# Performance work log

Measured on AMD Instinct MI355X. Metric: run time of the kernel, lower is better.

## Reference

```python
import jax, jax.numpy as jnp
import numpy as np

T, B, DG, DH, S = 48, 96, 192, 384, 3
LAM, ETA = 0.9, 0.5
LN_EPS = 1e-5

def layernorm(x, g, b):
    m = jnp.mean(x, axis=-1, keepdims=True)
    v = jnp.var(x, axis=-1, keepdims=True)
    return (x - m) * jax.lax.rsqrt(v + LN_EPS) * g + b

def setup_inputs() -> dict:
    key = jax.random.key(0)
    k0, k1, k2, k3 = jax.random.split(key, 4)
    z_seq = jax.random.normal(k0, (T, B, DG), jnp.float32)
    # kaiming-uniform-ish / xavier-ish scaling for realism
    W_h = jax.random.normal(k1, (DH, DH), jnp.float32) * (2.0 / DH) ** 0.5
    W_g = jax.random.normal(k2, (DH, DG), jnp.float32) * (1.0 / DG) ** 0.5
    b_h = jnp.zeros((DH,), jnp.float32)
    ln_g = jnp.ones((DH,), jnp.float32)
    ln_b = jnp.zeros((DH,), jnp.float32)
    alpha_fw = jax.random.uniform(k3, (1,), jnp.float32)  # cfg.alpha_fw (learned scalar)
    return dict(z_seq=z_seq, W_h=W_h, W_g=W_g, b_h=b_h, ln_g=ln_g, ln_b=ln_b, alpha_fw=alpha_fw)

def reference(z_seq, W_h, W_g, b_h, ln_g, ln_b, alpha_fw):
    # compute_k(): curvature of cosine gate
    k = jnp.where(alpha_fw >= 0,
                  1.0 + jax.nn.softplus(alpha_fw),
                  1.0 / (1.0 + jax.nn.softplus(-alpha_fw)))  # shape (1,)

    def step(carry, z_t):
        h, A = carry                                   # h: [B,DH], A: [B,DH,DH]
        h_base = h @ W_h.T + z_t @ W_g.T + b_h          # [B,DH]
        h_s = jax.nn.relu(layernorm(h_base, ln_g, ln_b))
        # inner fast-weight settling loop with cosine-similarity gate
        for _ in range(S):
            Ah = jnp.einsum('bij,bj->bi', A, h_s)       # bmm(A, h)
            dot = jnp.sum(h_s * Ah, axis=-1, keepdims=True)
            n1 = jnp.maximum(jnp.linalg.norm(h_s, axis=-1, keepdims=True), 1e-6)
            n2 = jnp.maximum(jnp.linalg.norm(Ah, axis=-1, keepdims=True), 1e-6)
            R = jnp.clip(dot / (n1 * n2), 0.0, 1.0)
            a = 1.0 - (1.0 - R) ** k                    # alpha_dyn, [B,1]
            h_s = jax.nn.relu(layernorm((1.0 - a * a) * h_base + a * Ah, ln_g, ln_b))
        h = h_s
        # Hebbian fast-weight update: A <- lambda*A + eta * h h^T
        A = LAM * A + ETA * jnp.einsum('bi,bj->bij', h, h)
        return (h, A), None

    Bn, Dh = z_seq.shape[1], W_h.shape[0]
    h0 = jnp.zeros((Bn, Dh), z_seq.dtype)
    A0 = jnp.zeros((Bn, Dh, Dh), z_seq.dtype)
    (h, A), _ = jax.lax.scan(step, (h0, A0), z_seq[:-1])

    # final (query) step: no gating, no A update, h_s = relu(LN(h_base + A h_s))
    z_t = z_seq[-1]
    h_base = h @ W_h.T + z_t @ W_g.T + b_h
    h = jax.nn.relu(layernorm(h_base, ln_g, ln_b))
    for _ in range(S):
        Ah = jnp.einsum('bij,bj->bi', A, h)
        h = jax.nn.relu(layernorm(h_base + Ah, ln_g, ln_b))
    return h
```

## Files before the change

kernel.cpp:

```cpp
#include <hip/hip_runtime.h>
#include <math.h>

#define TT    48
#define BB    96
#define DG    192
#define DH    384
#define NSTEP 47
#define SETI  3
#define NT    512
#define NWAVE 8
#define NOW   6
#define NG    32
#define RPG   12
#define PREPNT 768

typedef unsigned short ushort_t;
typedef float f32x2 __attribute__((ext_vector_type(2)));

template <int CTRL, int RM>
__device__ __forceinline__ float dppadd(float acc, float x) {
  int t = __builtin_amdgcn_update_dpp(0, __float_as_int(x), CTRL, RM, 0xF, false);
  return acc + __int_as_float(t);
}

__device__ __forceinline__ float row16_sum(float v) {
  v = dppadd<0x128, 0xF>(v, v);
  v = dppadd<0x124, 0xF>(v, v);
  v = dppadd<0x122, 0xF>(v, v);
  v = dppadd<0x121, 0xF>(v, v);
  return v;
}

__device__ __forceinline__ float wave_sum63(float v) {
  v = row16_sum(v);
  v = dppadd<0x142, 0xA>(v, v);
  v = dppadd<0x143, 0xC>(v, v);
  return v;
}

__device__ __forceinline__ float blo(unsigned u) {
  return __uint_as_float(u << 16);
}
__device__ __forceinline__ float bhi(unsigned u) {
  return __uint_as_float(u & 0xFFFF0000u);
}
__device__ __forceinline__ f32x2 pkfma(f32x2 a, f32x2 b, f32x2 c) {
  return __builtin_elementwise_fma(a, b, c);
}

__device__ __forceinline__ void matvec_full(
    const ushort_t* __restrict__ Wh_b,
    const float* __restrict__ hs, const float* __restrict__ gzs,
    float* __restrict__ hbs, float& s1, float& s2,
    int g, int lane16, bool with_h)
{
  f32x2 h2[12];
  if (with_h) {
    const float4* h4 = (const float4*)hs;
#pragma unroll
    for (int c = 0; c < 6; ++c) {
      float4 hh = h4[lane16 + 16 * c];
      h2[2 * c]     = f32x2{hh.x, hh.y};
      h2[2 * c + 1] = f32x2{hh.z, hh.w};
    }
  }
#pragma unroll 2
  for (int p = 0; p < RPG; ++p) {
    const int r = g + NG * p;
    f32x2 a0 = {0.f, 0.f}, a1 = {0.f, 0.f};
    if (with_h) {
      const uint2* wh = (const uint2*)Wh_b + (size_t)r * (DH / 4);
#pragma unroll
      for (int c = 0; c < 6; ++c) {
        uint2 u = wh[lane16 + 16 * c];
        a0 = pkfma(f32x2{blo(u.x), bhi(u.x)}, h2[2 * c], a0);
        a1 = pkfma(f32x2{blo(u.y), bhi(u.y)}, h2[2 * c + 1], a1);
      }
    }
    float acc = row16_sum((a0.x + a1.x) + (a0.y + a1.y));
    if (lane16 == 0) {
      float vv = acc + gzs[r];
      hbs[r] = vv;
      s1 += vv;
      s2 += vv * vv;
    }
  }
}

__device__ __forceinline__ void matvec_ref(
    const float* __restrict__ Wh_f, const float* __restrict__ Wg_f,
    const float* __restrict__ hs, const float* __restrict__ zsh,
    const float (&bias)[RPG], float* __restrict__ hbs,
    float& s1, float& s2, int g, int lane16, bool with_h)
{
  f32x2 h2[12];
  if (with_h) {
    const float4* h4 = (const float4*)hs;
#pragma unroll
    for (int c = 0; c < 6; ++c) {
      float4 hh = h4[lane16 + 16 * c];
      h2[2 * c]     = f32x2{hh.x, hh.y};
      h2[2 * c + 1] = f32x2{hh.z, hh.w};
    }
  }
  float4 zz[3];
  const float4* z4 = (const float4*)zsh;
#pragma unroll
  for (int c = 0; c < 3; ++c) zz[c] = z4[lane16 + 16 * c];
#pragma unroll 2
  for (int p = 0; p < RPG; ++p) {
    const int r = g + NG * p;
    f32x2 a0 = {0.f, 0.f}, a1 = {0.f, 0.f};
    const float4* wg = (const float4*)Wg_f + (size_t)r * (DG / 4);
#pragma unroll
    for (int c = 0; c < 3; ++c) {
      float4 w = wg[lane16 + 16 * c];
      a0 = pkfma(f32x2{w.x, w.y}, f32x2{zz[c].x, zz[c].y}, a0);
      a1 = pkfma(f32x2{w.z, w.w}, f32x2{zz[c].z, zz[c].w}, a1);
    }
    if (with_h) {
      const float4* wh = (const float4*)Wh_f + (size_t)r * (DH / 4);
#pragma unroll
      for (int c = 0; c < 6; ++c) {
        float4 w = wh[lane16 + 16 * c];
        a0 = pkfma(f32x2{w.x, w.y}, h2[2 * c], a0);
        a1 = pkfma(f32x2{w.z, w.w}, h2[2 * c + 1], a1);
      }
    }
    float acc = row16_sum((a0.x + a1.x) + (a0.y + a1.y));
    if (lane16 == 0) {
      float vv = acc + bias[p];
      hbs[r] = vv;
      s1 += vv;
      s2 += vv * vv;
    }
  }
}

template <bool FULL>
__global__ __launch_bounds__(NT, 2) void fw_rnn_kernel(
    const float* __restrict__ z_seq,
    const float* __restrict__ Wh_f,
    const float* __restrict__ Wg_f,
    const ushort_t* __restrict__ Wh_b,
    const float* __restrict__ gz,
    const float* __restrict__ b_h,
    const float* __restrict__ ln_g,
    const float* __restrict__ ln_b,
    const float* __restrict__ alpha_fw,
    float* __restrict__ out)
{
  __shared__ __align__(16) float hs[DH];
  __shared__ __align__(16) float hbs[DH];
  __shared__ __align__(16) float gzs[DH];
  __shared__ __align__(16) float zsh[DG];
  __shared__ float wlam[NSTEP];
  __shared__ __align__(16) float carr[48];
  __shared__ __align__(16) float redA[NWAVE * 2];
  __shared__ __align__(16) float redB[2][32];

  const int tid    = threadIdx.x;
  const int b      = blockIdx.x;
  const int lane   = tid & 63, wv = tid >> 6;
  const int g      = tid >> 4, lane16 = tid & 15;
  const bool owner = (tid < DH);
  const bool zst   = (!FULL) && (tid >= DH) && (tid < DH + DG / 4);

  float bias[RPG];
#pragma unroll
  for (int p = 0; p < RPG; ++p) bias[p] = 0.f;
  if (!FULL && lane16 == 0) {
#pragma unroll
    for (int p = 0; p < RPG; ++p) bias[p] = b_h[g + NG * p];
  }
  float g_i = 0.f, be_i = 0.f;
  if (owner) { g_i = ln_g[tid]; be_i = ln_b[tid]; }

  const float af   = alpha_fw[0];
  const float kcur = (af >= 0.f) ? (1.f + log1pf(expf(af)))
                                 : (1.f / (1.f + log1pf(expf(-af))));
  const float invD = 1.0f / (float)DH;

  float hcol[48];
#pragma unroll
  for (int q = 0; q < 48; ++q) hcol[q] = 0.f;
  float4 hregA[6], hregB[6];
#pragma unroll
  for (int c = 0; c < 6; ++c) {
    hregA[c] = float4{0.f, 0.f, 0.f, 0.f};
    hregB[c] = float4{0.f, 0.f, 0.f, 0.f};
  }

  if (FULL && tid < DH / 4)
    ((float4*)gzs)[tid] = ((const float4*)(gz + (size_t)b * DH))[tid];
  if (!FULL && tid < DG / 4)
    ((float4*)zsh)[tid] = ((const float4*)(z_seq + (size_t)b * DG))[tid];
  if (tid < 48) carr[tid] = 0.f;
  if (tid < 2) { redB[tid][30] = 0.f; redB[tid][31] = 0.f; }
  __syncthreads();

  float Shb = 0.f, Shb2 = 0.f;

  for (int t = 0; t < NSTEP; ++t) {
    float4 gzn = {0.f, 0.f, 0.f, 0.f};
    if (FULL && tid < DH / 4)
      gzn = ((const float4*)(gz + ((size_t)(t + 1) * BB + b) * DH))[tid];

    float s1 = 0.f, s2 = 0.f;
    if (FULL)
      matvec_full(Wh_b, hs, gzs, hbs, s1, s2, g, lane16, t > 0);
    else
      matvec_ref(Wh_f, Wg_f, hs, zsh, bias, hbs, s1, s2, g, lane16, t > 0);

    if (t > 0) {
      if (g == t - 1) {
#pragma unroll
        for (int c = 0; c < 6; ++c) hregA[c] = ((const float4*)hs)[lane16 + 16 * c];
      }
      if (g + NG == t - 1) {
#pragma unroll
        for (int c = 0; c < 6; ++c) hregB[c] = ((const float4*)hs)[lane16 + 16 * c];
      }
    }
    {
      float v0 = wave_sum63(s1);
      float v1 = wave_sum63(s2);
      if (lane == 63) { redA[wv * 2] = v0; redA[wv * 2 + 1] = v1; }
    }
    __syncthreads();

    float hb = 0.f, hsv = 0.f;
    if (owner) {
      float S1 = 0.f, S2 = 0.f;
      const float4* ra4 = (const float4*)redA;
#pragma unroll
      for (int q = 0; q < 4; ++q) {
        float4 ch = ra4[q];
        S1 += ch.x + ch.z;
        S2 += ch.y + ch.w;
      }
      Shb = S1; Shb2 = S2;
      hb = hbs[tid];
      float m   = S1 * invD;
      float var = S2 * invD - m * m;
      hsv = fmaxf((hb - m) * rsqrtf(var + 1e-5f) * g_i + be_i, 0.f);
      hs[tid] = hsv;
    }
    if (t == 0) {
      if (owner) hcol[0] = hsv;
      if (tid == 0) wlam[0] = 0.5f;
      if (FULL && tid < DH / 4) ((float4*)gzs)[tid] = gzn;
      if (zst)
        ((float4*)zsh)[tid - DH] =
            ((const float4*)(z_seq + ((size_t)1 * BB + b) * DG))[tid - DH];
      __syncthreads();
      continue;
    }
    __syncthreads();

    float4 znext;
    if (zst)
      znext = ((const float4*)(z_seq + ((size_t)(t + 1) * BB + b) * DG))[tid - DH];

    for (int s = 0; s < SETI; ++s) {
      if (g < t) {
        float4 ss[6];
        const float4* s4 = (const float4*)hs;
#pragma unroll
        for (int c = 0; c < 6; ++c) ss[c] = s4[lane16 + 16 * c];
        {
          f32x2 p0 = {0.f, 0.f}, p1 = {0.f, 0.f};
#pragma unroll
          for (int c = 0; c < 6; ++c) {
            p0 = pkfma(f32x2{hregA[c].x, hregA[c].y}, f32x2{ss[c].x, ss[c].y}, p0);
            p1 = pkfma(f32x2{hregA[c].z, hregA[c].w}, f32x2{ss[c].z, ss[c].w}, p1);
          }
          float p = row16_sum((p0.x + p1.x) + (p0.y + p1.y));
          if (lane16 == 0) carr[g] = p * wlam[g];
        }
        if (g + NG < t) {
          f32x2 p0 = {0.f, 0.f}, p1 = {0.f, 0.f};
#pragma unroll
          for (int c = 0; c < 6; ++c) {
            p0 = pkfma(f32x2{hregB[c].x, hregB[c].y}, f32x2{ss[c].x, ss[c].y}, p0);
            p1 = pkfma(f32x2{hregB[c].z, hregB[c].w}, f32x2{ss[c].z, ss[c].w}, p1);
          }
          float p = row16_sum((p0.x + p1.x) + (p0.y + p1.y));
          if (lane16 == 0) carr[g + NG] = p * wlam[g + NG];
        }
      }
      __syncthreads();

      float ah = 0.f;
      if (owner) {
        const float4* c4 = (const float4*)carr;
        float a0 = 0.f, a1 = 0.f, a2 = 0.f, a3 = 0.f;
#pragma unroll
        for (int q = 0; q < 12; ++q) {
          float4 cc = c4[q];
          a0 = fmaf(cc.x, hcol[4 * q + 0], a0);
          a1 = fmaf(cc.y, hcol[4 * q + 1], a1);
          a2 = fmaf(cc.z, hcol[4 * q + 2], a2);
          a3 = fmaf(cc.w, hcol[4 * q + 3], a3);
        }
        ah = (a0 + a2) + (a1 + a3);
        float v0 = wave_sum63(hsv * ah);
        float v1 = wave_sum63(hsv * hsv);
        float v2 = wave_sum63(ah * ah);
        float v3 = wave_sum63(hb * ah);
        float v4 = wave_sum63(ah);
        if (lane == 63) {
          float* rb = redB[s & 1];
          rb[wv * 5 + 0] = v0; rb[wv * 5 + 1] = v1; rb[wv * 5 + 2] = v2;
          rb[wv * 5 + 3] = v3; rb[wv * 5 + 4] = v4;
        }
      }
      __syncthreads();

      if (owner) {
        const float4* rb4 = (const float4*)redB[s & 1];
        float S[5] = {0.f, 0.f, 0.f, 0.f, 0.f};
#pragma unroll
        for (int q = 0; q < 8; ++q) {
          float4 ch = rb4[q];
          S[(4 * q + 0) % 5] += ch.x;
          S[(4 * q + 1) % 5] += ch.y;
          S[(4 * q + 2) % 5] += ch.z;
          S[(4 * q + 3) % 5] += ch.w;
        }
        float n1 = fmaxf(sqrtf(S[1]), 1e-6f);
        float n2 = fmaxf(sqrtf(S[2]), 1e-6f);
        float R  = fminf(fmaxf(__fdividef(S[0], n1 * n2), 0.f), 1.f);
        float a  = 1.f - __expf(kcur * __logf(1.f - R));
        float beta = 1.f - a * a;
        float mu  = (beta * Shb + a * S[4]) * invD;
        float Exx = (beta * beta * Shb2 + 2.f * beta * a * S[3] + a * a * S[2]) * invD;
        float var = Exx - mu * mu;
        float xv  = beta * hb + a * ah;
        hsv = fmaxf((xv - mu) * rsqrtf(var + 1e-5f) * g_i + be_i, 0.f);
        hs[tid] = hsv;
        if (s == SETI - 1) {
#pragma unroll
          for (int q = 0; q < 48; ++q)
            if (q == t) hcol[q] = hsv;
        }
      }
      if (s == SETI - 1) {
        if (tid < t) wlam[tid] *= 0.9f;
        else if (tid == t) wlam[tid] = 0.5f;
        if (FULL && tid < DH / 4) ((float4*)gzs)[tid] = gzn;
        if (zst) ((float4*)zsh)[tid - DH] = znext;
      }
      __syncthreads();
    }
  }

  {
    float s1 = 0.f, s2 = 0.f;
    if (FULL)
      matvec_full(Wh_b, hs, gzs, hbs, s1, s2, g, lane16, true);
    else
      matvec_ref(Wh_f, Wg_f, hs, zsh, bias, hbs, s1, s2, g, lane16, true);
    if (g + NG == NSTEP - 1) {
#pragma unroll
      for (int c = 0; c < 6; ++c) hregB[c] = ((const float4*)hs)[lane16 + 16 * c];
    }
    {
      float v0 = wave_sum63(s1);
      float v1 = wave_sum63(s2);
      if (lane == 63) { redA[wv * 2] = v0; redA[wv * 2 + 1] = v1; }
    }
    __syncthreads();

    float hb = 0.f, hv = 0.f;
    if (owner) {
      float S1 = 0.f, S2 = 0.f;
      const float4* ra4 = (const float4*)redA;
#pragma unroll
      for (int q = 0; q < 4; ++q) {
        float4 ch = ra4[q];
        S1 += ch.x + ch.z;
        S2 += ch.y + ch.w;
      }
      Shb = S1; Shb2 = S2;
      hb = hbs[tid];
      float m   = S1 * invD;
      float var = S2 * invD - m * m;
      hv = fmaxf((hb - m) * rsqrtf(var + 1e-5f) * g_i + be_i, 0.f);
      hs[tid] = hv;
    }
    __syncthreads();

    for (int s = 0; s < SETI; ++s) {
      {
        float4 ss[6];
        const float4* s4 = (const float4*)hs;
#pragma unroll
        for (int c = 0; c < 6; ++c) ss[c] = s4[lane16 + 16 * c];
        {
          f32x2 p0 = {0.f, 0.f}, p1 = {0.f, 0.f};
#pragma unroll
          for (int c = 0; c < 6; ++c) {
            p0 = pkfma(f32x2{hregA[c].x, hregA[c].y}, f32x2{ss[c].x, ss[c].y}, p0);
            p1 = pkfma(f32x2{hregA[c].z, hregA[c].w}, f32x2{ss[c].z, ss[c].w}, p1);
          }
          float p = row16_sum((p0.x + p1.x) + (p0.y + p1.y));
          if (lane16 == 0) carr[g] = p * wlam[g];
        }
        if (g + NG < NSTEP) {
          f32x2 p0 = {0.f, 0.f}, p1 = {0.f, 0.f};
#pragma unroll
          for (int c = 0; c < 6; ++c) {
            p0 = pkfma(f32x2{hregB[c].x, hregB[c].y}, f32x2{ss[c].x, ss[c].y}, p0);
            p1 = pkfma(f32x2{hregB[c].z, hregB[c].w}, f32x2{ss[c].z, ss[c].w}, p1);
          }
          float p = row16_sum((p0.x + p1.x) + (p0.y + p1.y));
          if (lane16 == 0) carr[g + NG] = p * wlam[g + NG];
        }
      }
      __syncthreads();

      float ah = 0.f;
      if (owner) {
        const float4* c4 = (const float4*)carr;
        float a0 = 0.f, a1 = 0.f, a2 = 0.f, a3 = 0.f;
#pragma unroll
        for (int q = 0; q < 12; ++q) {
          float4 cc = c4[q];
          a0 = fmaf(cc.x, hcol[4 * q + 0], a0);
          a1 = fmaf(cc.y, hcol[4 * q + 1], a1);
          a2 = fmaf(cc.z, hcol[4 * q + 2], a2);
          a3 = fmaf(cc.w, hcol[4 * q + 3], a3);
        }
        ah = (a0 + a2) + (a1 + a3);
        float v0 = wave_sum63(ah);
        float v1 = wave_sum63(ah * ah);
        float v2 = wave_sum63(hb * ah);
        if (lane == 63) {
          float* rb = redB[s & 1];
          rb[wv * 5 + 0] = v0; rb[wv * 5 + 1] = v1; rb[wv * 5 + 2] = v2;
        }
      }
      __syncthreads();

      if (owner) {
        const float4* rb4 = (const float4*)redB[s & 1];
        float S[5] = {0.f, 0.f, 0.f, 0.f, 0.f};
#pragma unroll
        for (int q = 0; q < 8; ++q) {
          float4 ch = rb4[q];
          S[(4 * q + 0) % 5] += ch.x;
          S[(4 * q + 1) % 5] += ch.y;
          S[(4 * q + 2) % 5] += ch.z;
          S[(4 * q + 3) % 5] += ch.w;
        }
        float Sx  = Shb + S[0];
        float Sxx = Shb2 + 2.f * S[2] + S[1];
        float mu  = Sx * invD;
        float var = Sxx * invD - mu * mu;
        float xv  = hb + ah;
        hv = fmaxf((xv - mu) * rsqrtf(var + 1e-5f) * g_i + be_i, 0.f);
        if (s < SETI - 1) hs[tid] = hv;
      }
      if (s < SETI - 1) __syncthreads();
    }

    if (owner) out[(size_t)b * DH + tid] = hv;
  }
}

__global__ __launch_bounds__(PREPNT) void prep_kernel(
    const float* __restrict__ z_seq, const float* __restrict__ Wg,
    const float* __restrict__ W_h, const float* __restrict__ b_h,
    ushort_t* __restrict__ Whb, float* __restrict__ gz)
{
  __shared__ __align__(16) float zsh[DG];
  const int tid = threadIdx.x, b = blockIdx.x;
  const int g = tid >> 4, lane16 = tid & 15;

  {
    int lid = (blockIdx.y * BB + blockIdx.x) * PREPNT + tid;
    if (lid < DH * DH) {
      unsigned u = __float_as_uint(W_h[lid]);
      unsigned r = (u + 0x7FFFu + ((u >> 16) & 1u)) >> 16;
      Whb[lid] = (ushort_t)r;
    }
  }

  float4 w[24];
#pragma unroll
  for (int p = 0; p < 8; ++p)
#pragma unroll
    for (int c = 0; c < 3; ++c)
      w[p * 3 + c] = ((const float4*)Wg)[(size_t)(8 * g + p) * (DG / 4) + lane16 + 16 * c];
  float4 bs0 = {0.f, 0.f, 0.f, 0.f}, bs1 = {0.f, 0.f, 0.f, 0.f};
  if (lane16 == 0) {
    bs0 = ((const float4*)b_h)[2 * g];
    bs1 = ((const float4*)b_h)[2 * g + 1];
  }
  for (int tt = 0; tt < 6; ++tt) {
    const int t = blockIdx.y * 6 + tt;
    __syncthreads();
    if (tid < DG / 4)
      ((float4*)zsh)[tid] = ((const float4*)(z_seq + ((size_t)t * BB + b) * DG))[tid];
    __syncthreads();
    float4 zz[3];
#pragma unroll
    for (int c = 0; c < 3; ++c) zz[c] = ((const float4*)zsh)[lane16 + 16 * c];
    float rs[8];
#pragma unroll
    for (int p = 0; p < 8; ++p) {
      f32x2 a0 = {0.f, 0.f}, a1 = {0.f, 0.f};
#pragma unroll
      for (int c = 0; c < 3; ++c) {
        a0 = pkfma(f32x2{w[p * 3 + c].x, w[p * 3 + c].y}, f32x2{zz[c].x, zz[c].y}, a0);
        a1 = pkfma(f32x2{w[p * 3 + c].z, w[p * 3 + c].w}, f32x2{zz[c].z, zz[c].w}, a1);
      }
      rs[p] = row16_sum((a0.x + a1.x) + (a0.y + a1.y));
    }
    if (lane16 == 0) {
      float* grow = gz + ((size_t)t * BB + b) * DH + 8 * g;
      ((float4*)grow)[0] = float4{rs[0] + bs0.x, rs[1] + bs0.y, rs[2] + bs0.z, rs[3] + bs0.w};
      ((float4*)grow)[1] = float4{rs[4] + bs1.x, rs[5] + bs1.y, rs[6] + bs1.z, rs[7] + bs1.w};
    }
  }
}

extern "C" void kernel_launch(void* const* d_in, const int* in_sizes, int n_in,
                              void* d_out, int out_size, void* d_ws, size_t ws_size,
                              hipStream_t stream) {
  const float* z_seq    = (const float*)d_in[0];
  const float* W_h      = (const float*)d_in[1];
  const float* W_g      = (const float*)d_in[2];
  const float* b_h      = (const float*)d_in[3];
  const float* ln_g     = (const float*)d_in[4];
  const float* ln_b     = (const float*)d_in[5];
  const float* alpha_fw = (const float*)d_in[6];
  float* out = (float*)d_out;

  const size_t nWh = (size_t)DH * DH;
  const size_t bf16Bytes = nWh * sizeof(ushort_t);
  const size_t gzBytes   = (size_t)TT * BB * DH * sizeof(float);

  if (ws_size >= bf16Bytes + gzBytes) {
    ushort_t* Whb = (ushort_t*)d_ws;
    float* gz = (float*)((char*)d_ws + bf16Bytes);
    prep_kernel<<<dim3(BB, 8), dim3(PREPNT), 0, stream>>>(
        z_seq, W_g, W_h, b_h, Whb, gz);
    fw_rnn_kernel<true><<<dim3(BB), dim3(NT), 0, stream>>>(
        z_seq, W_h, W_g, Whb, gz, b_h, ln_g, ln_b, alpha_fw, out);
  } else {
    fw_rnn_kernel<false><<<dim3(BB), dim3(NT), 0, stream>>>(
        z_seq, W_h, W_g, nullptr, nullptr, b_h, ln_g, ln_b, alpha_fw, out);
  }
}
```

Before: 545.5 us.

## Stage half of bf16 W_h in LDS and prefetch the rest into registers

```diff
diff --git a/kernel.cpp b/kernel.cpp
--- a/kernel.cpp
+++ b/kernel.cpp
@@ -12,6 +12,8 @@
 #define NOW   6
 #define NG    32
 #define RPG   12
+#define LWROWS 192
+#define LWSTR  97
 #define PREPNT 768
 
 typedef unsigned short ushort_t;
@@ -48,14 +50,34 @@
   return __builtin_elementwise_fma(a, b, c);
 }
 
+__device__ __forceinline__ float rowdot(const uint2* w, const f32x2 (&h2)[12]) {
+  f32x2 a0 = {0.f, 0.f}, a1 = {0.f, 0.f};
+#pragma unroll
+  for (int c = 0; c < 6; ++c) {
+    uint2 u = w[c];
+    a0 = pkfma(f32x2{blo(u.x), bhi(u.x)}, h2[2 * c], a0);
+    a1 = pkfma(f32x2{blo(u.y), bhi(u.y)}, h2[2 * c + 1], a1);
+  }
+  return row16_sum((a0.x + a1.x) + (a0.y + a1.y));
+}
+
 __device__ __forceinline__ void matvec_full(
-    const ushort_t* __restrict__ Wh_b,
+    const uint2* __restrict__ lwh, const ushort_t* __restrict__ Wh_b,
     const float* __restrict__ hs, const float* __restrict__ gzs,
     float* __restrict__ hbs, float& s1, float& s2,
     int g, int lane16, bool with_h)
 {
-  f32x2 h2[12];
+  float rs[RPG];
   if (with_h) {
+    const uint2* wsrc = (const uint2*)Wh_b;
+    uint2 uwA[18];
+#pragma unroll
+    for (int pp = 0; pp < 3; ++pp)
+#pragma unroll
+      for (int c = 0; c < 6; ++c)
+        uwA[pp * 6 + c] =
+            wsrc[(size_t)(g + NG * (6 + pp)) * (DH / 4) + lane16 + 16 * c];
+    f32x2 h2[12];
     const float4* h4 = (const float4*)hs;
 #pragma unroll
     for (int c = 0; c < 6; ++c) {
@@ -63,23 +85,40 @@
       h2[2 * c]     = f32x2{hh.x, hh.y};
       h2[2 * c + 1] = f32x2{hh.z, hh.w};
     }
-  }
-#pragma unroll 2
-  for (int p = 0; p < RPG; ++p) {
-    const int r = g + NG * p;
-    f32x2 a0 = {0.f, 0.f}, a1 = {0.f, 0.f};
-    if (with_h) {
-      const uint2* wh = (const uint2*)Wh_b + (size_t)r * (DH / 4);
+#pragma unroll
+    for (int p = 0; p < 6; ++p) {
+      const int r = g + NG * p;
+      f32x2 a0 = {0.f, 0.f}, a1 = {0.f, 0.f};
 #pragma unroll
       for (int c = 0; c < 6; ++c) {
-        uint2 u = wh[lane16 + 16 * c];
+        uint2 u = lwh[r * LWSTR + lane16 + 16 * c];
         a0 = pkfma(f32x2{blo(u.x), bhi(u.x)}, h2[2 * c], a0);
         a1 = pkfma(f32x2{blo(u.y), bhi(u.y)}, h2[2 * c + 1], a1);
       }
-    }
-    float acc = row16_sum((a0.x + a1.x) + (a0.y + a1.y));
-    if (lane16 == 0) {
-      float vv = acc + gzs[r];
+      rs[p] = row16_sum((a0.x + a1.x) + (a0.y + a1.y));
+    }
+    uint2 uwB[18];
+#pragma unroll
+    for (int pp = 0; pp < 3; ++pp)
+#pragma unroll
+      for (int c = 0; c < 6; ++c)
+        uwB[pp * 6 + c] =
+            wsrc[(size_t)(g + NG * (9 + pp)) * (DH / 4) + lane16 + 16 * c];
+    rs[6] = rowdot(uwA, h2);
+    rs[7] = rowdot(uwA + 6, h2);
+    rs[8] = rowdot(uwA + 12, h2);
+    rs[9]  = rowdot(uwB, h2);
+    rs[10] = rowdot(uwB + 6, h2);
+    rs[11] = rowdot(uwB + 12, h2);
+  } else {
+#pragma unroll
+    for (int p = 0; p < RPG; ++p) rs[p] = 0.f;
+  }
+  if (lane16 == 0) {
+#pragma unroll
+    for (int p = 0; p < RPG; ++p) {
+      const int r = g + NG * p;
+      float vv = rs[p] + gzs[r];
       hbs[r] = vv;
       s1 += vv;
       s2 += vv * vv;
@@ -150,6 +189,7 @@
     const float* __restrict__ alpha_fw,
     float* __restrict__ out)
 {
+  __shared__ __align__(16) uint2 lwh[LWROWS * LWSTR];
   __shared__ __align__(16) float hs[DH];
   __shared__ __align__(16) float hbs[DH];
   __shared__ __align__(16) float gzs[DH];
@@ -166,6 +206,14 @@
   const bool owner = (tid < DH);
   const bool zst   = (!FULL) && (tid >= DH) && (tid < DH + DG / 4);
 
+  if (FULL) {
+    const uint2* src = (const uint2*)Wh_b;
+    for (int i = tid; i < LWROWS * 96; i += NT) {
+      int row = i / 96, col = i - 96 * (i / 96);
+      lwh[row * LWSTR + col] = src[(size_t)row * 96 + col];
+    }
+  }
+
   float bias[RPG];
 #pragma unroll
   for (int p = 0; p < RPG; ++p) bias[p] = 0.f;
@@ -208,7 +256,7 @@
 
     float s1 = 0.f, s2 = 0.f;
     if (FULL)
-      matvec_full(Wh_b, hs, gzs, hbs, s1, s2, g, lane16, t > 0);
+      matvec_full(lwh, Wh_b, hs, gzs, hbs, s1, s2, g, lane16, t > 0);
     else
       matvec_ref(Wh_f, Wg_f, hs, zsh, bias, hbs, s1, s2, g, lane16, t > 0);
 
@@ -358,7 +406,7 @@
   {
     float s1 = 0.f, s2 = 0.f;
     if (FULL)
-      matvec_full(Wh_b, hs, gzs, hbs, s1, s2, g, lane16, true);
+      matvec_full(lwh, Wh_b, hs, gzs, hbs, s1, s2, g, lane16, true);
     else
       matvec_ref(Wh_f, Wg_f, hs, zsh, bias, hbs, s1, s2, g, lane16, true);
     if (g + NG == NSTEP - 1) {
```

Result: faster. 525.1 us (-3.7%).
